# Kernel optimization log

Measured on AMD Instinct MI355X. Metric: run time of the kernel, lower is better.

## Reference

```python
import jax, jax.numpy as jnp
import numpy as np

B, T, C, H = 8, 2048, 384, 64

def setup_inputs() -> dict:
    key = jax.random.key(0)
    k1, k2, k3, k4 = jax.random.split(key, 4)
    x = jax.random.normal(k1, (B, T, C), dtype=jnp.float32)
    Wq = jax.random.normal(k2, (C, H), dtype=jnp.float32) * (C ** -0.5)
    Wk = jax.random.normal(k3, (C, H), dtype=jnp.float32) * (C ** -0.5)
    Wv = jax.random.normal(k4, (C, H), dtype=jnp.float32) * (C ** -0.5)
    return {"x": x, "Wq": Wq, "Wk": Wk, "Wv": Wv}

def reference(x, Wq, Wk, Wv):
    # x: (B, T, C); projections: (B, T, H)
    Bn, Tn, Cn = x.shape
    q = jnp.einsum('btc,ch->bth', x, Wq)
    k = jnp.einsum('btc,ch->bth', x, Wk)
    v = jnp.einsum('btc,ch->bth', x, Wv)
    # NOTE: source scales by C**-0.5 (embedding dim), not head_size**-0.5
    weights = jnp.einsum('bth,bsh->bts', q, k) * (Cn ** -0.5)  # (B, T, T)
    causal = jnp.tril(jnp.ones((Tn, Tn), dtype=bool))
    weights = jnp.where(causal, weights, -jnp.inf)
    # NOTE: source applies softmax over dim=1 (query/row axis), reproduced faithfully
    weights = jax.nn.softmax(weights, axis=1)
    # dropout omitted (eval-mode reference)
    return jnp.einsum('bts,bsh->bth', weights, v)
```

## Files before the change

kernel.cpp:

```cpp
#include <hip/hip_runtime.h>
#include <hip/hip_bf16.h>
#include <math.h>

#define Bn 8
#define Tn 2048
#define Cn 384
#define Hn 64
#define SCALE 0.051031036307982884f

using bf16x8 = __attribute__((ext_vector_type(8))) short;
using f32x4  = __attribute__((ext_vector_type(4))) float;

#define MFMA(a, b, c) __builtin_amdgcn_mfma_f32_16x16x32_bf16((a), (b), (c), 0, 0, 0)

static __device__ __forceinline__ short f2bf(float f) {
  unsigned u = __float_as_uint(f);
  u += 0x7fffu + ((u >> 16) & 1u);
  return (short)(u >> 16);
}

__global__ __launch_bounds__(256) void wconv_kernel(
    const float* __restrict__ Wq, const float* __restrict__ Wk,
    const float* __restrict__ Wv, short* __restrict__ WbT) {
  int idx = blockIdx.x * 256 + threadIdx.x;
  int n = idx / 384, k = idx - n * 384;
  const float* W = (n < 64) ? Wq : (n < 128) ? Wk : Wv;
  WbT[idx] = f2bf(W[k * 64 + (n & 63)]);
}

__global__ __launch_bounds__(256) void proj_kernel(
    const float* __restrict__ x, const short* __restrict__ WbT,
    short* __restrict__ qb, short* __restrict__ kb, short* __restrict__ vT) {
  __shared__ short xs[16][392];
  __shared__ short vtile[64][20];
  const int tid = threadIdx.x;
  const int t0 = blockIdx.x * 16;
  const float* xb = x + (size_t)t0 * Cn;
  #pragma unroll
  for (int i = 0; i < 6; ++i) {
    int j = tid + i * 256;
    int row = j / 96, colv = (j - row * 96) * 4;
    float4 v = *(const float4*)(xb + row * Cn + colv);
    short4 s4; s4.x = f2bf(v.x); s4.y = f2bf(v.y); s4.z = f2bf(v.z); s4.w = f2bf(v.w);
    *(short4*)(&xs[row][colv]) = s4;
  }
  __syncthreads();
  const int w = tid >> 6, l15 = tid & 15, quad = (tid & 63) >> 4;
  f32x4 acc[3] = {};
  for (int ks = 0; ks < 12; ++ks) {
    bf16x8 a = *(const bf16x8*)(&xs[l15][ks * 32 + quad * 8]);
    #pragma unroll
    for (int cf = 0; cf < 3; ++cf) {
      bf16x8 bfr = *(const bf16x8*)(WbT + (size_t)(48 * w + 16 * cf + l15) * Cn + ks * 32 + quad * 8);
      acc[cf] = MFMA(a, bfr, acc[cf]);
    }
  }
  #pragma unroll
  for (int cf = 0; cf < 3; ++cf) {
    int cbase = 48 * w + 16 * cf, c = cbase + l15;
    #pragma unroll
    for (int r = 0; r < 4; ++r) {
      int row = t0 + quad * 4 + r;
      short val = f2bf(acc[cf][r]);
      if (cbase < 64)       qb[(size_t)row * Hn + c] = val;
      else if (cbase < 128) kb[(size_t)row * Hn + (c - 64)] = val;
      else                  vtile[c - 128][quad * 4 + r] = val;
    }
  }
  __syncthreads();
  const int b = t0 >> 11, t0l = t0 & 2047;
  int h = tid >> 2, tseg = (tid & 3) * 4;
  *(short4*)(vT + ((size_t)(b * Hn + h)) * Tn + t0l + tseg) =
      *(const short4*)(&vtile[h][tseg]);
}

__global__ __launch_bounds__(256) void colstats_kernel(
    const short* __restrict__ qb, const short* __restrict__ kb,
    float* __restrict__ L) {
  const int unit = blockIdx.x;
  const int b = unit >> 7, rem = unit & 127;
  const int j = rem >> 3, u = rem & 7;
  const int lo = (u * 33) >> 3, hi = ((u + 1) * 33) >> 3;
  const int big = 32 - j;
  const int tid = threadIdx.x, w = tid >> 6, l15 = tid & 15, quad = (tid & 63) >> 4;
  __shared__ float redl[64][17];

  auto run = [&](const int i, const int k0, const int k1) {
    if (k0 >= k1) return;
    const int s0 = i << 6;
    bf16x8 bk[8];
    #pragma unroll
    for (int nf = 0; nf < 4; ++nf) {
      const size_t krow = (size_t)(b * Tn + s0 + 16 * nf + l15) * Hn;
      bk[2 * nf]     = *(const bf16x8*)(kb + krow + quad * 8);
      bk[2 * nf + 1] = *(const bf16x8*)(kb + krow + 32 + quad * 8);
    }
    float l[4] = {0.f, 0.f, 0.f, 0.f};
    auto cload = [&](bf16x8& A0, bf16x8& A1, int k) {
      size_t ar = (size_t)(b * Tn + ((i + k) << 6) + 16 * w + l15) * Hn;
      A0 = *(const bf16x8*)(qb + ar + quad * 8);
      A1 = *(const bf16x8*)(qb + ar + 32 + quad * 8);
    };
    auto ccomp = [&](bf16x8 A0, bf16x8 A1, int k) {
      f32x4 sc[4] = {};
      #pragma unroll
      for (int nf = 0; nf < 4; ++nf) {
        sc[nf] = MFMA(A0, bk[2 * nf], sc[nf]);
        sc[nf] = MFMA(A1, bk[2 * nf + 1], sc[nf]);
      }
      const bool diag = (k == 0);
      const int tb = ((i + k) << 6) + 16 * w + quad * 4;
      #pragma unroll
      for (int nf = 0; nf < 4; ++nf) {
        int s = s0 + 16 * nf + l15;
        #pragma unroll
        for (int r = 0; r < 4; ++r) {
          float v = sc[nf][r] * SCALE;
          if (diag && (tb + r) < s) v = -INFINITY;
          l[nf] += __expf(v);
        }
      }
    };
    bf16x8 a0A, a1A, a0B, a1B;
    cload(a0A, a1A, k0);
    int k = k0;
    while (k + 1 < k1) {
      cload(a0B, a1B, k + 1);
      ccomp(a0A, a1A, k);
      if (k + 2 < k1) cload(a0A, a1A, k + 2);
      ccomp(a0B, a1B, k + 1);
      k += 2;
    }
    if (k < k1) ccomp(a0A, a1A, k);
    __syncthreads();
    #pragma unroll
    for (int nf = 0; nf < 4; ++nf) redl[16 * nf + l15][w * 4 + quad] = l[nf];
    __syncthreads();
    if (tid < 64) {
      float ls = 0.f;
      #pragma unroll
      for (int q2 = 0; q2 < 16; ++q2) ls += redl[tid][q2];
      atomicAdd(&L[b * Tn + s0 + tid], ls);
    }
  };
  run(j, lo, min(hi, big));
  run(31 - j, max(lo, big) - big, hi - big);
}

__global__ __launch_bounds__(256) void inv_kernel(
    const float* __restrict__ L, float* __restrict__ lL) {
  int gid = blockIdx.x * 256 + threadIdx.x;
  lL[gid] = 1.0f / L[gid];
}

__global__ __launch_bounds__(256) void outp_kernel(
    const short* __restrict__ qb, const short* __restrict__ kb,
    const short* __restrict__ vT, const float* __restrict__ lL,
    float* __restrict__ out) {
  const int unit = blockIdx.x;
  const int b = unit >> 7, rem = unit & 127;
  const int j = rem >> 3, u = rem & 7;
  const int lo = (u * 33) >> 3, hi = ((u + 1) * 33) >> 3;
  const int big = 32 - j;
  const int tid = threadIdx.x, w = tid >> 6, l15 = tid & 15, quad = (tid & 63) >> 4;
  __shared__ short P[4][16][72];

  auto run = [&](const int tile, const int k0, const int k1) {
    if (k0 >= k1) return;
    const int tr = (tile << 6) + 16 * w;
    const size_t qrow = (size_t)(b * Tn + tr + l15) * Hn;
    bf16x8 aq0 = *(const bf16x8*)(qb + qrow + quad * 8);
    bf16x8 aq1 = *(const bf16x8*)(qb + qrow + 32 + quad * 8);
    f32x4 acc[4] = {};
    bf16x8 kA[8], vA[8], kB[8], vB[8];
    float rlA[4], rlB[4];
    auto load = [&](bf16x8 (&kk)[8], bf16x8 (&vv)[8], float (&rl)[4], int ch) {
      const int s0 = ch << 6;
      #pragma unroll
      for (int nf = 0; nf < 4; ++nf) {
        const size_t krow = (size_t)(b * Tn + s0 + 16 * nf + l15) * Hn;
        kk[2 * nf]     = *(const bf16x8*)(kb + krow + quad * 8);
        kk[2 * nf + 1] = *(const bf16x8*)(kb + krow + 32 + quad * 8);
        const size_t vrow = (size_t)(b * Hn + 16 * nf + l15) * Tn + s0;
        vv[2 * nf]     = *(const bf16x8*)(vT + vrow + quad * 8);
        vv[2 * nf + 1] = *(const bf16x8*)(vT + vrow + 32 + quad * 8);
        rl[nf] = lL[b * Tn + s0 + 16 * nf + l15];
      }
    };
    auto comp = [&](bf16x8 (&kk)[8], bf16x8 (&vv)[8], float (&rl)[4], int ch) {
      f32x4 sc[4] = {};
      #pragma unroll
      for (int nf = 0; nf < 4; ++nf) {
        sc[nf] = MFMA(aq0, kk[2 * nf], sc[nf]);
        sc[nf] = MFMA(aq1, kk[2 * nf + 1], sc[nf]);
      }
      const int s0 = ch << 6;
      const bool diagc = (ch == tile);
      #pragma unroll
      for (int nf = 0; nf < 4; ++nf) {
        int s = s0 + 16 * nf + l15;
        #pragma unroll
        for (int r = 0; r < 4; ++r) {
          float wgt = __expf(sc[nf][r] * SCALE) * rl[nf];
          if (diagc && s > tr + quad * 4 + r) wgt = 0.f;
          P[w][quad * 4 + r][16 * nf + l15] = f2bf(wgt);
        }
      }
      bf16x8 ap0 = *(const bf16x8*)(&P[w][l15][quad * 8]);
      bf16x8 ap1 = *(const bf16x8*)(&P[w][l15][32 + quad * 8]);
      #pragma unroll
      for (int nf = 0; nf < 4; ++nf) {
        acc[nf] = MFMA(ap0, vv[2 * nf], acc[nf]);
        acc[nf] = MFMA(ap1, vv[2 * nf + 1], acc[nf]);
      }
    };
    load(kA, vA, rlA, k0);
    int ch = k0;
    while (ch + 1 < k1) {
      load(kB, vB, rlB, ch + 1);
      comp(kA, vA, rlA, ch);
      if (ch + 2 < k1) load(kA, vA, rlA, ch + 2);
      comp(kB, vB, rlB, ch + 1);
      ch += 2;
    }
    if (ch < k1) comp(kA, vA, rlA, ch);
    #pragma unroll
    for (int nf = 0; nf < 4; ++nf)
      #pragma unroll
      for (int r = 0; r < 4; ++r)
        atomicAdd(&out[(size_t)(b * Tn + tr + quad * 4 + r) * Hn + 16 * nf + l15],
                  acc[nf][r]);
  };
  run(31 - j, lo, min(hi, big));
  run(j, max(lo, big) - big, hi - big);
}

extern "C" void kernel_launch(void* const* d_in, const int* in_sizes, int n_in,
                              void* d_out, int out_size, void* d_ws, size_t ws_size,
                              hipStream_t stream) {
  const float* x  = (const float*)d_in[0];
  const float* Wq = (const float*)d_in[1];
  const float* Wk = (const float*)d_in[2];
  const float* Wv = (const float*)d_in[3];
  char* ws = (char*)d_ws;
  short* qb   = (short*)(ws);
  short* kb   = (short*)(ws + 2097152);
  short* vT   = (short*)(ws + 4194304);
  short* WbT  = (short*)(ws + 6291456);
  float* L    = (float*)(ws + 6438912);
  float* lL   = (float*)(ws + 6504448);
  float* outp = (float*)d_out;

  hipMemsetAsync(L, 0, (size_t)Bn * Tn * 4, stream);
  hipMemsetAsync(outp, 0, (size_t)Bn * Tn * Hn * 4, stream);
  hipLaunchKernelGGL(wconv_kernel, dim3(288), dim3(256), 0, stream, Wq, Wk, Wv, WbT);
  hipLaunchKernelGGL(proj_kernel, dim3(Bn * Tn / 16), dim3(256), 0, stream, x, WbT, qb, kb, vT);
  hipLaunchKernelGGL(colstats_kernel, dim3(1024), dim3(256), 0, stream, qb, kb, L);
  hipLaunchKernelGGL(inv_kernel, dim3(64), dim3(256), 0, stream, L, lL);
  hipLaunchKernelGGL(outp_kernel, dim3(1024), dim3(256), 0, stream, qb, kb, vT, lL, outp);
}
```

Before: 156.8 us.

## Materialize exp score matrix and replace recompute pass with plain GEMM

The column-statistics kernel now also writes every exponentiated causal score to a bf16 B×T×T buffer in workspace. The per-key normalization moves into V: a new kernel divides V^T by the column sums, so the output pass becomes a straightforward E·V̂ GEMM with direct stores. This drops the second QK^T, the second exp pass and the output atomics, along with the output memset. In exchange it adds tens of megabytes of scattered 2-byte global stores and reads, and launches only 256 output blocks with heavily unbalanced per-tile work.

After: 153.8 us. No clear change (-1.9%).

```diff
diff --git a/kernel.cpp b/kernel.cpp
--- a/kernel.cpp
+++ b/kernel.cpp
@@ -17,6 +17,9 @@
   unsigned u = __float_as_uint(f);
   u += 0x7fffu + ((u >> 16) & 1u);
   return (short)(u >> 16);
+}
+static __device__ __forceinline__ float bf2f(short s) {
+  return __uint_as_float(((unsigned)(unsigned short)s) << 16);
 }
 
 __global__ __launch_bounds__(256) void wconv_kernel(
@@ -76,13 +79,14 @@
 
 __global__ __launch_bounds__(256) void colstats_kernel(
     const short* __restrict__ qb, const short* __restrict__ kb,
-    float* __restrict__ L) {
+    float* __restrict__ L, short* __restrict__ Eb) {
   const int unit = blockIdx.x;
   const int b = unit >> 7, rem = unit & 127;
   const int j = rem >> 3, u = rem & 7;
   const int lo = (u * 33) >> 3, hi = ((u + 1) * 33) >> 3;
   const int big = 32 - j;
   const int tid = threadIdx.x, w = tid >> 6, l15 = tid & 15, quad = (tid & 63) >> 4;
+  const size_t Ebase = (size_t)b * Tn * Tn;
   __shared__ float redl[64][17];
 
   auto run = [&](const int i, const int k0, const int k1) {
@@ -117,7 +121,9 @@
         for (int r = 0; r < 4; ++r) {
           float v = sc[nf][r] * SCALE;
           if (diag && (tb + r) < s) v = -INFINITY;
-          l[nf] += __expf(v);
+          float ev = __expf(v);
+          l[nf] += ev;
+          Eb[Ebase + (size_t)(tb + r) * Tn + s] = f2bf(ev);
         }
       }
     };
@@ -147,92 +153,71 @@
   run(31 - j, max(lo, big) - big, hi - big);
 }
 
-__global__ __launch_bounds__(256) void inv_kernel(
-    const float* __restrict__ L, float* __restrict__ lL) {
+__global__ __launch_bounds__(256) void vhat_kernel(
+    const short* __restrict__ vT, const float* __restrict__ L,
+    short* __restrict__ vS) {
   int gid = blockIdx.x * 256 + threadIdx.x;
-  lL[gid] = 1.0f / L[gid];
-}
-
-__global__ __launch_bounds__(256) void outp_kernel(
-    const short* __restrict__ qb, const short* __restrict__ kb,
-    const short* __restrict__ vT, const float* __restrict__ lL,
+  size_t base = (size_t)gid * 8;
+  int b = (int)(base >> 17), s = (int)(base & 2047);
+  short4 v0 = *(const short4*)(vT + base);
+  short4 v1 = *(const short4*)(vT + base + 4);
+  const float* Lp = L + b * Tn + s;
+  float4 L0 = *(const float4*)(Lp);
+  float4 L1 = *(const float4*)(Lp + 4);
+  short4 r0, r1;
+  r0.x = f2bf(bf2f(v0.x) / L0.x); r0.y = f2bf(bf2f(v0.y) / L0.y);
+  r0.z = f2bf(bf2f(v0.z) / L0.z); r0.w = f2bf(bf2f(v0.w) / L0.w);
+  r1.x = f2bf(bf2f(v1.x) / L1.x); r1.y = f2bf(bf2f(v1.y) / L1.y);
+  r1.z = f2bf(bf2f(v1.z) / L1.z); r1.w = f2bf(bf2f(v1.w) / L1.w);
+  *(short4*)(vS + base) = r0;
+  *(short4*)(vS + base + 4) = r1;
+}
+
+__global__ __launch_bounds__(256) void outg_kernel(
+    const short* __restrict__ Eb, const short* __restrict__ vS,
     float* __restrict__ out) {
-  const int unit = blockIdx.x;
-  const int b = unit >> 7, rem = unit & 127;
-  const int j = rem >> 3, u = rem & 7;
-  const int lo = (u * 33) >> 3, hi = ((u + 1) * 33) >> 3;
-  const int big = 32 - j;
+  const int g = blockIdx.x;
+  const int tile = 31 - (g >> 3), b = g & 7;
   const int tid = threadIdx.x, w = tid >> 6, l15 = tid & 15, quad = (tid & 63) >> 4;
-  __shared__ short P[4][16][72];
-
-  auto run = [&](const int tile, const int k0, const int k1) {
-    if (k0 >= k1) return;
-    const int tr = (tile << 6) + 16 * w;
-    const size_t qrow = (size_t)(b * Tn + tr + l15) * Hn;
-    bf16x8 aq0 = *(const bf16x8*)(qb + qrow + quad * 8);
-    bf16x8 aq1 = *(const bf16x8*)(qb + qrow + 32 + quad * 8);
-    f32x4 acc[4] = {};
-    bf16x8 kA[8], vA[8], kB[8], vB[8];
-    float rlA[4], rlB[4];
-    auto load = [&](bf16x8 (&kk)[8], bf16x8 (&vv)[8], float (&rl)[4], int ch) {
-      const int s0 = ch << 6;
-      #pragma unroll
-      for (int nf = 0; nf < 4; ++nf) {
-        const size_t krow = (size_t)(b * Tn + s0 + 16 * nf + l15) * Hn;
-        kk[2 * nf]     = *(const bf16x8*)(kb + krow + quad * 8);
-        kk[2 * nf + 1] = *(const bf16x8*)(kb + krow + 32 + quad * 8);
-        const size_t vrow = (size_t)(b * Hn + 16 * nf + l15) * Tn + s0;
-        vv[2 * nf]     = *(const bf16x8*)(vT + vrow + quad * 8);
-        vv[2 * nf + 1] = *(const bf16x8*)(vT + vrow + 32 + quad * 8);
-        rl[nf] = lL[b * Tn + s0 + 16 * nf + l15];
-      }
-    };
-    auto comp = [&](bf16x8 (&kk)[8], bf16x8 (&vv)[8], float (&rl)[4], int ch) {
-      f32x4 sc[4] = {};
-      #pragma unroll
-      for (int nf = 0; nf < 4; ++nf) {
-        sc[nf] = MFMA(aq0, kk[2 * nf], sc[nf]);
-        sc[nf] = MFMA(aq1, kk[2 * nf + 1], sc[nf]);
-      }
-      const int s0 = ch << 6;
-      const bool diagc = (ch == tile);
-      #pragma unroll
-      for (int nf = 0; nf < 4; ++nf) {
-        int s = s0 + 16 * nf + l15;
-        #pragma unroll
-        for (int r = 0; r < 4; ++r) {
-          float wgt = __expf(sc[nf][r] * SCALE) * rl[nf];
-          if (diagc && s > tr + quad * 4 + r) wgt = 0.f;
-          P[w][quad * 4 + r][16 * nf + l15] = f2bf(wgt);
-        }
-      }
-      bf16x8 ap0 = *(const bf16x8*)(&P[w][l15][quad * 8]);
-      bf16x8 ap1 = *(const bf16x8*)(&P[w][l15][32 + quad * 8]);
-      #pragma unroll
-      for (int nf = 0; nf < 4; ++nf) {
-        acc[nf] = MFMA(ap0, vv[2 * nf], acc[nf]);
-        acc[nf] = MFMA(ap1, vv[2 * nf + 1], acc[nf]);
-      }
-    };
-    load(kA, vA, rlA, k0);
-    int ch = k0;
-    while (ch + 1 < k1) {
-      load(kB, vB, rlB, ch + 1);
-      comp(kA, vA, rlA, ch);
-      if (ch + 2 < k1) load(kA, vA, rlA, ch + 2);
-      comp(kB, vB, rlB, ch + 1);
-      ch += 2;
-    }
-    if (ch < k1) comp(kA, vA, rlA, ch);
-    #pragma unroll
-    for (int nf = 0; nf < 4; ++nf)
-      #pragma unroll
-      for (int r = 0; r < 4; ++r)
-        atomicAdd(&out[(size_t)(b * Tn + tr + quad * 4 + r) * Hn + 16 * nf + l15],
-                  acc[nf][r]);
+  const int tbase = (tile << 6) + 16 * w;
+  const size_t Abase = (size_t)b * Tn * Tn + (size_t)(tbase + l15) * Tn;
+  const size_t Bbase = (size_t)b * Hn * Tn;
+  f32x4 acc[4] = {};
+  const int nch = tile + 1;
+  bf16x8 aA[2], bA[8], aB[2], bB[8];
+  auto load = [&](bf16x8 (&A)[2], bf16x8 (&Bf)[8], int ch) {
+    const int s0 = ch << 6;
+    A[0] = *(const bf16x8*)(Eb + Abase + s0 + quad * 8);
+    A[1] = *(const bf16x8*)(Eb + Abase + s0 + 32 + quad * 8);
+    #pragma unroll
+    for (int nf = 0; nf < 4; ++nf) {
+      const size_t br = Bbase + (size_t)(16 * nf + l15) * Tn + s0;
+      Bf[2 * nf]     = *(const bf16x8*)(vS + br + quad * 8);
+      Bf[2 * nf + 1] = *(const bf16x8*)(vS + br + 32 + quad * 8);
+    }
   };
-  run(31 - j, lo, min(hi, big));
-  run(j, max(lo, big) - big, hi - big);
+  auto comp = [&](bf16x8 (&A)[2], bf16x8 (&Bf)[8]) {
+    #pragma unroll
+    for (int nf = 0; nf < 4; ++nf) {
+      acc[nf] = MFMA(A[0], Bf[2 * nf], acc[nf]);
+      acc[nf] = MFMA(A[1], Bf[2 * nf + 1], acc[nf]);
+    }
+  };
+  load(aA, bA, 0);
+  int ch = 0;
+  while (ch + 1 < nch) {
+    load(aB, bB, ch + 1);
+    comp(aA, bA);
+    if (ch + 2 < nch) load(aA, bA, ch + 2);
+    comp(aB, bB);
+    ch += 2;
+  }
+  if (ch < nch) comp(aA, bA);
+  #pragma unroll
+  for (int nf = 0; nf < 4; ++nf)
+    #pragma unroll
+    for (int r = 0; r < 4; ++r)
+      out[(size_t)(b * Tn + tbase + quad * 4 + r) * Hn + 16 * nf + l15] = acc[nf][r];
 }
 
 extern "C" void kernel_launch(void* const* d_in, const int* in_sizes, int n_in,
@@ -246,16 +231,16 @@
   short* qb   = (short*)(ws);
   short* kb   = (short*)(ws + 2097152);
   short* vT   = (short*)(ws + 4194304);
-  short* WbT  = (short*)(ws + 6291456);
-  float* L    = (float*)(ws + 6438912);
-  float* lL   = (float*)(ws + 6504448);
+  short* vS   = (short*)(ws + 6291456);
+  short* WbT  = (short*)(ws + 8388608);
+  float* L    = (float*)(ws + 8536064);
+  short* Eb   = (short*)(ws + 16777216);
   float* outp = (float*)d_out;
 
   hipMemsetAsync(L, 0, (size_t)Bn * Tn * 4, stream);
-  hipMemsetAsync(outp, 0, (size_t)Bn * Tn * Hn * 4, stream);
   hipLaunchKernelGGL(wconv_kernel, dim3(288), dim3(256), 0, stream, Wq, Wk, Wv, WbT);
   hipLaunchKernelGGL(proj_kernel, dim3(Bn * Tn / 16), dim3(256), 0, stream, x, WbT, qb, kb, vT);
-  hipLaunchKernelGGL(colstats_kernel, dim3(1024), dim3(256), 0, stream, qb, kb, L);
-  hipLaunchKernelGGL(inv_kernel, dim3(64), dim3(256), 0, stream, L, lL);
-  hipLaunchKernelGGL(outp_kernel, dim3(1024), dim3(256), 0, stream, qb, kb, vT, lL, outp);
-}
+  hipLaunchKernelGGL(colstats_kernel, dim3(1024), dim3(256), 0, stream, qb, kb, L, Eb);
+  hipLaunchKernelGGL(vhat_kernel, dim3(512), dim3(256), 0, stream, vT, L, vS);
+  hipLaunchKernelGGL(outg_kernel, dim3(256), dim3(256), 0, stream, Eb, vS, outp);
+}
```
